# Kernel tuning notes

Hardware: AMD Instinct MI355X
Metric: run time of the kernel (lower is better)

## Reference

```python
import jax, jax.numpy as jnp
import numpy as np

T, HID, D, NQ, NKV = 4096, 2048, 128, 16, 4
THETA = 10000.0


def _rope(x, pos):
    # x: [T, N, D], non-interleaved (rotate_half) RoPE
    half = D // 2
    inv_freq = 1.0 / (THETA ** (jnp.arange(0, half, dtype=jnp.float32) / half))
    freqs = pos.astype(jnp.float32)[:, None] * inv_freq[None, :]  # [T, half]
    cos = jnp.cos(freqs)[:, None, :]  # [T, 1, half]
    sin = jnp.sin(freqs)[:, None, :]
    x1, x2 = x[..., :half], x[..., half:]
    return jnp.concatenate([x1 * cos - x2 * sin, x2 * cos + x1 * sin], axis=-1)


def setup_inputs() -> dict:
    key = jax.random.key(0)
    ks = jax.random.split(key, 5)
    s = 0.02
    return {
        "hidden_states": jax.random.normal(ks[0], (T, HID), jnp.float32),
        "wq": jax.random.normal(ks[1], (HID, HID), jnp.float32) * s,
        "wk": jax.random.normal(ks[2], (NKV * D, HID), jnp.float32) * s,
        "wv": jax.random.normal(ks[3], (NKV * D, HID), jnp.float32) * s,
        "wo": jax.random.normal(ks[4], (HID, HID), jnp.float32) * s,
        "position_ids": jnp.arange(T, dtype=jnp.int32),
    }


def reference(hidden_states, wq, wk, wv, wo, position_ids):
    q = (hidden_states @ wq.T).reshape(T, NQ, D)
    k = (hidden_states @ wk.T).reshape(T, NKV, D)
    v = (hidden_states @ wv.T).reshape(T, NKV, D)
    q = _rope(q, position_ids)
    k = _rope(k, position_ids)
    # GQA: share each KV head across NQ//NKV query heads
    rep = NQ // NKV
    k = jnp.repeat(k, rep, axis=1)  # [T, NQ, D]
    v = jnp.repeat(v, rep, axis=1)
    scale = 1.0 / jnp.sqrt(jnp.float32(D))
    scores = jnp.einsum("qhd,khd->hqk", q, k) * scale  # [NQ, T, T]
    causal = jnp.tril(jnp.ones((T, T), dtype=bool))
    scores = jnp.where(causal[None, :, :], scores, jnp.float32(-1e30))
    probs = jax.nn.softmax(scores, axis=-1)
    out = jnp.einsum("hqk,khd->qhd", probs, v).reshape(T, HID)
    return out @ wo.T
```

## Files before the change

### kernel.cpp

```cpp
#include <hip/hip_runtime.h>
#include <hip/hip_bf16.h>
#include <cstdint>

#define T_    4096
#define HID_  2048
#define DH    128
#define NQ_   16
#define NKV_  4
#define QKVW  3072

typedef __attribute__((ext_vector_type(8))) short bf16x8;
typedef __attribute__((ext_vector_type(4))) float f32x4;
typedef __attribute__((ext_vector_type(16))) float f32x16;
typedef __attribute__((ext_vector_type(4))) float f4;
typedef __attribute__((ext_vector_type(4))) short s4;

__device__ __forceinline__ short f2bf(float f) {
  union { float f; unsigned u; } x; x.f = f;
  unsigned r = x.u + 0x7fffu + ((x.u >> 16) & 1u);
  return (short)(r >> 16);
}
__device__ __forceinline__ float bf2f(short s) {
  return __uint_as_float(((unsigned)(unsigned short)s) << 16);
}
__device__ __forceinline__ unsigned pkbf2(float a, float b) {
  union { __hip_bfloat162 h; unsigned u; } c;
  c.h = __float22bfloat162_rn(make_float2(a, b));
  return c.u;
}

__device__ __forceinline__ void gload16(const void* g, void* l) {
  __builtin_amdgcn_global_load_lds(
      (const __attribute__((address_space(1))) unsigned*)g,
      (__attribute__((address_space(3))) unsigned*)l, 16, 0, 0);
}

#define MFMA16(a, b, c) __builtin_amdgcn_mfma_f32_16x16x32_bf16(a, b, c, 0, 0, 0)
#define MFMA32(a, b, c) __builtin_amdgcn_mfma_f32_32x32x16_bf16(a, b, c, 0, 0, 0)

#define Z16 {0.f,0.f,0.f,0.f,0.f,0.f,0.f,0.f,0.f,0.f,0.f,0.f,0.f,0.f,0.f,0.f}
#define SCL2 0.127517432f

#define C_HS 2097152u
#define C_WQ (C_HS + 1048576u)
#define C_WK (C_WQ + 262144u)
#define C_WV (C_WK + 262144u)
#define C_WO (C_WV + 1048576u)
__global__ void cvt_all(const float* __restrict__ hs, const float* __restrict__ wq,
                        const float* __restrict__ wk, const float* __restrict__ wv,
                        const float* __restrict__ wo, short* __restrict__ hs_bf,
                        short* __restrict__ w1_bf, short* __restrict__ wo_bf) {
  const unsigned stride = gridDim.x * blockDim.x;
  for (unsigned i = blockIdx.x * blockDim.x + threadIdx.x; i < C_WO; i += stride) {
    const float* s; short* d; unsigned off;
    if (i < C_HS)      { s = hs; d = hs_bf;           off = i; }
    else if (i < C_WQ) { s = wq; d = w1_bf;           off = i - C_HS; }
    else if (i < C_WK) { s = wk; d = w1_bf + 4194304; off = i - C_WQ; }
    else if (i < C_WV) { s = wv; d = w1_bf + 5242880; off = i - C_WK; }
    else               { s = wo; d = wo_bf;           off = i - C_WV; }
    f4 v = ((const f4*)s)[off];
    s4 o;
    o[0] = f2bf(v[0]); o[1] = f2bf(v[1]); o[2] = f2bf(v[2]); o[3] = f2bf(v[3]);
    ((s4*)d)[off] = o;
  }
}

template <int BF16OUT>
__global__ __launch_bounds__(256) void gemm_bt(const short* __restrict__ A,
                                               const short* __restrict__ B,
                                               void* __restrict__ Cp,
                                               int N, int K) {
  __shared__ short lA[128 * 64];
  __shared__ short lB[128 * 64];
  const int nb = gridDim.x * gridDim.y;
  const int lin = blockIdx.y * gridDim.x + blockIdx.x;
  const int per = nb >> 3;
  const int wg = (lin & 7) * per + (lin >> 3);
  const int bx = wg % gridDim.x;
  const int by = wg / gridDim.x;

  const int tid = threadIdx.x;
  const int lane = tid & 63;
  const int w = tid >> 6;
  const int wr = w >> 1, wc = w & 1;
  const int l15 = lane & 15, l4 = lane >> 4;
  f32x4 acc[4][4];
#pragma unroll
  for (int m = 0; m < 4; m++)
#pragma unroll
    for (int n = 0; n < 4; n++) acc[m][n] = f32x4{0.f, 0.f, 0.f, 0.f};

  const short* Ag = A + (size_t)bx * 128 * K;
  const short* Bg = B + (size_t)by * 128 * K;

  for (int kt = 0; kt < K; kt += 64) {
#pragma unroll
    for (int i = 0; i < 4; ++i) {
      const int cb = i * 256 + w * 64;
      const int c = cb + lane;
      const int row = c >> 3;
      const int x = (c & 7) << 4;
      const int sx = x ^ ((row & 7) << 4);
      gload16(Ag + (size_t)row * K + kt + (sx >> 1), (char*)lA + cb * 16);
      gload16(Bg + (size_t)row * K + kt + (sx >> 1), (char*)lB + cb * 16);
    }
    __syncthreads();
    bf16x8 af[4][2], bfr[4][2];
#pragma unroll
    for (int m = 0; m < 4; m++) {
      const int row = wr * 64 + m * 16 + l15;
      const int sw = (row & 7) << 4;
#pragma unroll
      for (int kk = 0; kk < 2; kk++)
        af[m][kk] = *(const bf16x8*)((const char*)lA + row * 128 + ((kk * 64 + l4 * 16) ^ sw));
    }
#pragma unroll
    for (int n = 0; n < 4; n++) {
      const int row = wc * 64 + n * 16 + l15;
      const int sw = (row & 7) << 4;
#pragma unroll
      for (int kk = 0; kk < 2; kk++)
        bfr[n][kk] = *(const bf16x8*)((const char*)lB + row * 128 + ((kk * 64 + l4 * 16) ^ sw));
    }
#pragma unroll
    for (int m = 0; m < 4; m++)
#pragma unroll
      for (int n = 0; n < 4; n++) {
        acc[m][n] = MFMA16(af[m][0], bfr[n][0], acc[m][n]);
        acc[m][n] = MFMA16(af[m][1], bfr[n][1], acc[m][n]);
      }
    __syncthreads();
  }

  const int r0 = bx * 128 + wr * 64;
  const int c0 = by * 128 + wc * 64;
#pragma unroll
  for (int m = 0; m < 4; m++)
#pragma unroll
    for (int n = 0; n < 4; n++)
#pragma unroll
      for (int r = 0; r < 4; r++) {
        const int row = r0 + m * 16 + l4 * 4 + r;
        const int col = c0 + n * 16 + l15;
        if (BF16OUT)
          ((short*)Cp)[(size_t)row * N + col] = f2bf(acc[m][n][r]);
        else
          ((float*)Cp)[(size_t)row * N + col] = acc[m][n][r];
      }
}

__global__ void rope_k(short* __restrict__ qkv, const int* __restrict__ pos) {
  __shared__ float cs[64], sn[64];
  const int row = blockIdx.x;
  const int tid = threadIdx.x;
  if (tid < 64) {
    const float fp = (float)pos[row];
    const float freq = fp * powf(10000.0f, -(float)tid * (1.0f / 64.0f));
    cs[tid] = cosf(freq);
    sn[tid] = sinf(freq);
  }
  __syncthreads();
  const int p = tid * 4;
  const int head = p >> 6;
  const int d0 = p & 63;
  const int col0 = (head < NQ_) ? head * DH : HID_ + (head - NQ_) * DH;
  const float scl = (head < NQ_) ? SCL2 : 1.0f;
  short* q = qkv + (size_t)row * QKVW + col0 + d0;
  s4 x1 = *(const s4*)q;
  s4 x2 = *(const s4*)(q + 64);
  s4 o1, o2;
#pragma unroll
  for (int j = 0; j < 4; j++) {
    const float c = cs[d0 + j], s = sn[d0 + j];
    const float a = bf2f(x1[j]), b = bf2f(x2[j]);
    o1[j] = f2bf((a * c - b * s) * scl);
    o2[j] = f2bf((b * c + a * s) * scl);
  }
  *(s4*)q = o1;
  *(s4*)(q + 64) = o2;
}

#define PRE(j)                                                                      \
  {                                                                                 \
    const int kv0e = (j) * 128, kv0o = (j) * 128 + 64;                              \
    _Pragma("unroll") for (int i = 0; i < 2; i++) {                                 \
      const int idx = i * 512 + tid;                                                \
      const int row = idx >> 4, e = (idx & 15) << 3;                                \
      kre[i] = *(const bf16x8*)(kbase + (size_t)(kv0e + row) * QKVW + e);           \
      kro[i] = *(const bf16x8*)(kbase + (size_t)(kv0o + row) * QKVW + e);           \
    }                                                                               \
    {                                                                               \
      const int rp = tid >> 4, e = (tid & 15) << 3;                                 \
      vre[0] = *(const bf16x8*)(vbase + (size_t)(kv0e + 2 * rp) * QKVW + e);        \
      vre[1] = *(const bf16x8*)(vbase + (size_t)(kv0e + 2 * rp + 1) * QKVW + e);    \
      vro[0] = *(const bf16x8*)(vbase + (size_t)(kv0o + 2 * rp) * QKVW + e);        \
      vro[1] = *(const bf16x8*)(vbase + (size_t)(kv0o + 2 * rp + 1) * QKVW + e);    \
    }                                                                               \
  }

#define WRITEBUF(bufp)                                                          \
  {                                                                             \
    char* sKe_ = (bufp);                                                        \
    char* sKo_ = (bufp) + 16384;                                                \
    char* sVe_ = (bufp) + 32768;                                                \
    char* sVo_ = (bufp) + 49152;                                                \
    _Pragma("unroll") for (int i = 0; i < 2; i++) {                             \
      const int idx = i * 512 + tid;                                            \
      const int row = idx >> 4, e16 = (idx & 15) << 4;                          \
      const int swz = (((row >> 3) ^ row) & 7) << 4;                            \
      *(bf16x8*)(sKe_ + row * 256 + (e16 ^ swz)) = kre[i];                      \
      *(bf16x8*)(sKo_ + row * 256 + (e16 ^ swz)) = kro[i];                      \
    }                                                                           \
    {                                                                           \
      const int rp = tid >> 4, e = (tid & 15) << 3;                             \
      const int rp2 = (rp & ~6) | ((rp & 2) << 1) | ((rp & 4) >> 1);            \
      _Pragma("unroll") for (int jj = 0; jj < 8; jj++) {                        \
        const int d = e + jj;                                                   \
        const int swz = (((d >> 3) ^ d) & 7) << 4;                              \
        const unsigned pe = ((unsigned)(unsigned short)vre[0][jj]) |            \
                            (((unsigned)(unsigned short)vre[1][jj]) << 16);     \
        const unsigned po = ((unsigned)(unsigned short)vro[0][jj]) |            \
                            (((unsigned)(unsigned short)vro[1][jj]) << 16);     \
        *(unsigned*)(sVe_ + d * 128 + ((rp2 * 4) ^ swz)) = pe;                  \
        *(unsigned*)(sVo_ + d * 128 + ((rp2 * 4) ^ swz)) = po;                  \
      }                                                                         \
    }                                                                           \
  }

__global__ __launch_bounds__(512) void attn_k(const short* __restrict__ qkv,
                                              short* __restrict__ aout) {
  __shared__ __align__(16) char smem[67584];
  float* ml = (float*)(smem + 65536);

  const int lin = blockIdx.x;
  const int xcd = lin & 7;
  const int slot = lin >> 3;
  const int kvh = xcd >> 1;
  const int qb = 127 - (slot * 2 + (xcd & 1));
  const int tid = threadIdx.x, lane = tid & 63, w = tid >> 6;
  const int head = w & 3, sp = w >> 2;
  const int hi = lane >> 5, l31 = lane & 31;
  const int h = kvh * 4 + head;

  const short* kbase = qkv + HID_ + kvh * DH;
  const short* vbase = qkv + HID_ + NKV_ * DH + kvh * DH;
  const int spoff = sp ? 16384 : 0;

  const int qrow0 = qb * 32;
  const int ntiles = qb / 2 + 1;
  const int nsuper = (ntiles + 1) >> 1;
  const int myq = qrow0 + l31;

  bf16x8 qf[8];
  {
    const short* qp = qkv + (size_t)myq * QKVW + h * DH + hi * 8;
#pragma unroll
    for (int c = 0; c < 8; c++) qf[c] = *(const bf16x8*)(qp + c * 16);
  }
  f32x16 o[4] = {Z16, Z16, Z16, Z16};
  float m = -3e38f, l = 0.f;

  bf16x8 kre[2], kro[2], vre[2], vro[2];
  PRE(0)

  for (int j = 0; j < nsuper; ++j) {
    __syncthreads();
    WRITEBUF(smem)
    __syncthreads();
    if (j + 1 < nsuper) PRE(j + 1)
    const char* bK = smem + spoff;
    const char* bV = smem + 32768 + spoff;

    const int t = 2 * j + sp;
    if (t < ntiles) {
      const int kv0 = t * 64;
      f32x16 s0 = Z16, s1 = Z16;
      const int sw0 = (((l31 >> 3) ^ l31) & 7) << 4;
      const int r1 = 32 + l31;
      const int sw1 = (((r1 >> 3) ^ r1) & 7) << 4;
      __builtin_amdgcn_s_setprio(1);
#pragma unroll
      for (int c = 0; c < 8; c++) {
        const int co = c * 32 + hi * 16;
        const bf16x8 k0 = *(const bf16x8*)(bK + l31 * 256 + (co ^ sw0));
        const bf16x8 k1 = *(const bf16x8*)(bK + r1 * 256 + (co ^ sw1));
        s0 = MFMA32(k0, qf[c], s0);
        s1 = MFMA32(k1, qf[c], s1);
      }
      __builtin_amdgcn_s_setprio(0);
      float sv0[16], sv1[16];
      if (t == ntiles - 1) {
#pragma unroll
        for (int r = 0; r < 16; r++) {
          const int kk = (r & 3) + 8 * (r >> 2) + 4 * hi;
          sv0[r] = (kv0 + kk <= myq) ? s0[r] : -1e30f;
          sv1[r] = (kv0 + 32 + kk <= myq) ? s1[r] : -1e30f;
        }
      } else {
#pragma unroll
        for (int r = 0; r < 16; r++) {
          sv0[r] = s0[r];
          sv1[r] = s1[r];
        }
      }
      float mx[8];
#pragma unroll
      for (int r = 0; r < 8; r++)
        mx[r] = fmaxf(fmaxf(sv0[r], sv0[r + 8]), fmaxf(sv1[r], sv1[r + 8]));
#pragma unroll
      for (int st = 4; st > 0; st >>= 1)
#pragma unroll
        for (int r = 0; r < 4; r++)
          if (r < st) mx[r] = fmaxf(mx[r], mx[r + st]);
      float pm = fmaxf(mx[0], __shfl_xor(mx[0], 32));
      if (__any(pm > m + 11.5f)) {
        const float mn = fmaxf(m, pm);
        const float al = exp2f(m - mn);
        m = mn;
        l *= al;
#pragma unroll
        for (int r = 0; r < 16; r++) {
          const float ar = __shfl(al, (r & 3) + 8 * (r >> 2) + 4 * hi);
#pragma unroll
          for (int dt = 0; dt < 4; dt++) o[dt][r] *= ar;
        }
      }
      float pv0[16], pv1[16];
#pragma unroll
      for (int r = 0; r < 16; r++) {
        pv0[r] = exp2f(sv0[r] - m);
        pv1[r] = exp2f(sv1[r] - m);
      }
      float sum[8];
#pragma unroll
      for (int r = 0; r < 8; r++)
        sum[r] = (pv0[r] + pv0[r + 8]) + (pv1[r] + pv1[r + 8]);
#pragma unroll
      for (int st = 4; st > 0; st >>= 1)
#pragma unroll
        for (int r = 0; r < 4; r++)
          if (r < st) sum[r] = sum[r] + sum[r + st];
      l += sum[0] + __shfl_xor(sum[0], 32);

      unsigned W0[8], W1[8];
#pragma unroll
      for (int i = 0; i < 8; i++) {
        W0[i] = pkbf2(pv0[2 * i], pv0[2 * i + 1]);
        W1[i] = pkbf2(pv1[2 * i], pv1[2 * i + 1]);
      }
#pragma unroll
      for (int kt = 0; kt < 2; kt++) {
#pragma unroll
        for (int hc = 0; hc < 2; hc++) {
          union { unsigned u[4]; bf16x8 v; } fr;
#pragma unroll
          for (int mm = 0; mm < 4; mm++)
            fr.u[mm] = kt ? W1[hc * 4 + mm] : W0[hc * 4 + mm];
          const int ko = kt * 64 + hc * 32 + hi * 16;
          __builtin_amdgcn_s_setprio(1);
#pragma unroll
          for (int dt = 0; dt < 4; dt++) {
            const int row = dt * 32 + l31;
            const int swz = (((row >> 3) ^ row) & 7) << 4;
            const bf16x8 vf = *(const bf16x8*)(bV + row * 128 + (ko ^ swz));
            o[dt] = MFMA32(fr.v, vf, o[dt]);
          }
          __builtin_amdgcn_s_setprio(0);
        }
      }
    }
  }

  if (lane < 32) {
    ml[((head * 2 + sp) * 2) * 32 + lane] = m;
    ml[((head * 2 + sp) * 2 + 1) * 32 + lane] = l;
  }
  __syncthreads();
  const float mo = ml[((head * 2 + (1 - sp)) * 2) * 32 + l31];
  const float lo = ml[((head * 2 + (1 - sp)) * 2 + 1) * 32 + l31];
  const float M = fmaxf(m, mo);
  const float aown = exp2f(m - M);
  const float ltot = l * aown + lo * exp2f(mo - M);
#pragma unroll
  for (int r = 0; r < 16; r++) {
    const float ar = __shfl(aown, (r & 3) + 8 * (r >> 2) + 4 * hi);
#pragma unroll
    for (int dt = 0; dt < 4; dt++) o[dt][r] *= ar;
  }
  float* Ob = (float*)smem + head * 4096;
  if (sp == 1) {
#pragma unroll
    for (int r = 0; r < 16; r++) {
      const int q = (r & 3) + 8 * (r >> 2) + 4 * hi;
#pragma unroll
      for (int dt = 0; dt < 4; dt++) Ob[q * 128 + dt * 32 + l31] = o[dt][r];
    }
  }
  __syncthreads();
  if (sp == 0) {
    const float ri = 1.0f / ltot;
#pragma unroll
    for (int r = 0; r < 16; r++) {
      const float rr = __shfl(ri, (r & 3) + 8 * (r >> 2) + 4 * hi);
      const int q = (r & 3) + 8 * (r >> 2) + 4 * hi;
#pragma unroll
      for (int dt = 0; dt < 4; dt++) {
        const float val = (o[dt][r] + Ob[q * 128 + dt * 32 + l31]) * rr;
        aout[(size_t)(qrow0 + q) * HID_ + h * DH + dt * 32 + l31] = f2bf(val);
      }
    }
  }
}

extern "C" void kernel_launch(void* const* d_in, const int* in_sizes, int n_in,
                              void* d_out, int out_size, void* d_ws, size_t ws_size,
                              hipStream_t stream) {
  const float* hs = (const float*)d_in[0];
  const float* wq = (const float*)d_in[1];
  const float* wk = (const float*)d_in[2];
  const float* wv = (const float*)d_in[3];
  const float* wo = (const float*)d_in[4];
  const int* pos = (const int*)d_in[5];
  float* out = (float*)d_out;

  const size_t SZ_HS = (size_t)T_ * HID_;
  const size_t SZ_WQ = (size_t)HID_ * HID_;
  const size_t SZ_W1 = (size_t)QKVW * HID_;
  const size_t SZ_QKV = (size_t)T_ * QKVW;

  short* hs_bf = (short*)d_ws;
  short* w1_bf = hs_bf + SZ_HS;
  short* wo_bf = w1_bf + SZ_W1;
  short* qkv = wo_bf + SZ_WQ;
  short* attn = qkv + SZ_QKV;

  cvt_all<<<2048, 256, 0, stream>>>(hs, wq, wk, wv, wo, hs_bf, w1_bf, wo_bf);

  gemm_bt<1><<<dim3(T_ / 128, QKVW / 128), 256, 0, stream>>>(hs_bf, w1_bf, qkv, QKVW, HID_);

  rope_k<<<dim3(T_), 320, 0, stream>>>(qkv, pos);

  attn_k<<<dim3(512), 512, 0, stream>>>(qkv, attn);

  gemm_bt<0><<<dim3(T_ / 128, HID_ / 128), 256, 0, stream>>>(attn, wo_bf, out, HID_, HID_);
}
```

Baseline: 256.1 us.

## Drop split-KV within attention block; use 4 waves each iterating all KV tiles

Result: slower. 293.9 us (+14.7%).

```diff
diff --git a/kernel.cpp b/kernel.cpp
--- a/kernel.cpp
+++ b/kernel.cpp
@@ -180,36 +180,33 @@
   *(s4*)(q + 64) = o2;
 }
 
-#define PRE(j)                                                                      \
+
+#define PRE(tt)                                                                     \
   {                                                                                 \
-    const int kv0e = (j) * 128, kv0o = (j) * 128 + 64;                              \
-    _Pragma("unroll") for (int i = 0; i < 2; i++) {                                 \
-      const int idx = i * 512 + tid;                                                \
-      const int row = idx >> 4, e = (idx & 15) << 3;                                \
-      kre[i] = *(const bf16x8*)(kbase + (size_t)(kv0e + row) * QKVW + e);           \
-      kro[i] = *(const bf16x8*)(kbase + (size_t)(kv0o + row) * QKVW + e);           \
+    const int kv0p = (tt) * 64;                                                     \
+    _Pragma("unroll") for (int i = 0; i < 4; i++) {                                 \
+      const int c = i * 256 + tid;                                                  \
+      const int row = c >> 4, e = (c & 15) << 3;                                    \
+      kr[i] = *(const bf16x8*)(kbase + (size_t)(kv0p + row) * QKVW + e);            \
     }                                                                               \
     {                                                                               \
       const int rp = tid >> 4, e = (tid & 15) << 3;                                 \
-      vre[0] = *(const bf16x8*)(vbase + (size_t)(kv0e + 2 * rp) * QKVW + e);        \
-      vre[1] = *(const bf16x8*)(vbase + (size_t)(kv0e + 2 * rp + 1) * QKVW + e);    \
-      vro[0] = *(const bf16x8*)(vbase + (size_t)(kv0o + 2 * rp) * QKVW + e);        \
-      vro[1] = *(const bf16x8*)(vbase + (size_t)(kv0o + 2 * rp + 1) * QKVW + e);    \
+      vr[0] = *(const bf16x8*)(vbase + (size_t)(kv0p + 2 * rp) * QKVW + e);         \
+      vr[1] = *(const bf16x8*)(vbase + (size_t)(kv0p + 2 * rp + 1) * QKVW + e);     \
+      vr[2] = *(const bf16x8*)(vbase + (size_t)(kv0p + 2 * rp + 32) * QKVW + e);    \
+      vr[3] = *(const bf16x8*)(vbase + (size_t)(kv0p + 2 * rp + 33) * QKVW + e);    \
     }                                                                               \
   }
 
-#define WRITEBUF(bufp)                                                          \
+#define WRITEBUF()                                                              \
   {                                                                             \
-    char* sKe_ = (bufp);                                                        \
-    char* sKo_ = (bufp) + 16384;                                                \
-    char* sVe_ = (bufp) + 32768;                                                \
-    char* sVo_ = (bufp) + 49152;                                                \
-    _Pragma("unroll") for (int i = 0; i < 2; i++) {                             \
-      const int idx = i * 512 + tid;                                            \
-      const int row = idx >> 4, e16 = (idx & 15) << 4;                          \
+    char* sK_ = smem;                                                           \
+    char* sV_ = smem + 16384;                                                   \
+    _Pragma("unroll") for (int i = 0; i < 4; i++) {                             \
+      const int c = i * 256 + tid;                                              \
+      const int row = c >> 4, e16 = (c & 15) << 4;                              \
       const int swz = (((row >> 3) ^ row) & 7) << 4;                            \
-      *(bf16x8*)(sKe_ + row * 256 + (e16 ^ swz)) = kre[i];                      \
-      *(bf16x8*)(sKo_ + row * 256 + (e16 ^ swz)) = kro[i];                      \
+      *(bf16x8*)(sK_ + row * 256 + (e16 ^ swz)) = kr[i];                        \
     }                                                                           \
     {                                                                           \
       const int rp = tid >> 4, e = (tid & 15) << 3;                             \
@@ -217,38 +214,34 @@
       _Pragma("unroll") for (int jj = 0; jj < 8; jj++) {                        \
         const int d = e + jj;                                                   \
         const int swz = (((d >> 3) ^ d) & 7) << 4;                              \
-        const unsigned pe = ((unsigned)(unsigned short)vre[0][jj]) |            \
-                            (((unsigned)(unsigned short)vre[1][jj]) << 16);     \
-        const unsigned po = ((unsigned)(unsigned short)vro[0][jj]) |            \
-                            (((unsigned)(unsigned short)vro[1][jj]) << 16);     \
-        *(unsigned*)(sVe_ + d * 128 + ((rp2 * 4) ^ swz)) = pe;                  \
-        *(unsigned*)(sVo_ + d * 128 + ((rp2 * 4) ^ swz)) = po;                  \
+        const unsigned p0 = ((unsigned)(unsigned short)vr[0][jj]) |             \
+                            (((unsigned)(unsigned short)vr[1][jj]) << 16);      \
+        const unsigned p1 = ((unsigned)(unsigned short)vr[2][jj]) |             \
+                            (((unsigned)(unsigned short)vr[3][jj]) << 16);      \
+        *(unsigned*)(sV_ + d * 128 + ((rp2 * 4) ^ swz)) = p0;                   \
+        *(unsigned*)(sV_ + d * 128 + (((rp2 + 16) * 4) ^ swz)) = p1;            \
       }                                                                         \
     }                                                                           \
   }
 
-__global__ __launch_bounds__(512) void attn_k(const short* __restrict__ qkv,
+__global__ __launch_bounds__(256) void attn_k(const short* __restrict__ qkv,
                                               short* __restrict__ aout) {
-  __shared__ __align__(16) char smem[67584];
-  float* ml = (float*)(smem + 65536);
+  __shared__ __align__(16) char smem[32768];
 
   const int lin = blockIdx.x;
   const int xcd = lin & 7;
   const int slot = lin >> 3;
   const int kvh = xcd >> 1;
   const int qb = 127 - (slot * 2 + (xcd & 1));
-  const int tid = threadIdx.x, lane = tid & 63, w = tid >> 6;
-  const int head = w & 3, sp = w >> 2;
+  const int tid = threadIdx.x, lane = tid & 63, head = tid >> 6;
   const int hi = lane >> 5, l31 = lane & 31;
   const int h = kvh * 4 + head;
 
   const short* kbase = qkv + HID_ + kvh * DH;
   const short* vbase = qkv + HID_ + NKV_ * DH + kvh * DH;
-  const int spoff = sp ? 16384 : 0;
 
   const int qrow0 = qb * 32;
   const int ntiles = qb / 2 + 1;
-  const int nsuper = (ntiles + 1) >> 1;
   const int myq = qrow0 + l31;
 
   bf16x8 qf[8];
@@ -260,155 +253,122 @@
   f32x16 o[4] = {Z16, Z16, Z16, Z16};
   float m = -3e38f, l = 0.f;
 
-  bf16x8 kre[2], kro[2], vre[2], vro[2];
+  bf16x8 kr[4], vr[4];
   PRE(0)
 
-  for (int j = 0; j < nsuper; ++j) {
+  for (int t = 0; t < ntiles; ++t) {
     __syncthreads();
-    WRITEBUF(smem)
+    WRITEBUF()
     __syncthreads();
-    if (j + 1 < nsuper) PRE(j + 1)
-    const char* bK = smem + spoff;
-    const char* bV = smem + 32768 + spoff;
-
-    const int t = 2 * j + sp;
-    if (t < ntiles) {
-      const int kv0 = t * 64;
-      f32x16 s0 = Z16, s1 = Z16;
-      const int sw0 = (((l31 >> 3) ^ l31) & 7) << 4;
-      const int r1 = 32 + l31;
-      const int sw1 = (((r1 >> 3) ^ r1) & 7) << 4;
-      __builtin_amdgcn_s_setprio(1);
-#pragma unroll
-      for (int c = 0; c < 8; c++) {
-        const int co = c * 32 + hi * 16;
-        const bf16x8 k0 = *(const bf16x8*)(bK + l31 * 256 + (co ^ sw0));
-        const bf16x8 k1 = *(const bf16x8*)(bK + r1 * 256 + (co ^ sw1));
-        s0 = MFMA32(k0, qf[c], s0);
-        s1 = MFMA32(k1, qf[c], s1);
-      }
-      __builtin_amdgcn_s_setprio(0);
-      float sv0[16], sv1[16];
-      if (t == ntiles - 1) {
-#pragma unroll
-        for (int r = 0; r < 16; r++) {
-          const int kk = (r & 3) + 8 * (r >> 2) + 4 * hi;
-          sv0[r] = (kv0 + kk <= myq) ? s0[r] : -1e30f;
-          sv1[r] = (kv0 + 32 + kk <= myq) ? s1[r] : -1e30f;
+    if (t + 1 < ntiles) PRE(t + 1)
+    const char* bK = smem;
+    const char* bV = smem + 16384;
+    const int kv0 = t * 64;
+
+    f32x16 s0 = Z16, s1 = Z16;
+    const int sw0 = (((l31 >> 3) ^ l31) & 7) << 4;
+    const int r1 = 32 + l31;
+    const int sw1 = (((r1 >> 3) ^ r1) & 7) << 4;
+    __builtin_amdgcn_s_setprio(1);
+#pragma unroll
+    for (int c = 0; c < 8; c++) {
+      const int co = c * 32 + hi * 16;
+      const bf16x8 k0 = *(const bf16x8*)(bK + l31 * 256 + (co ^ sw0));
+      const bf16x8 k1 = *(const bf16x8*)(bK + r1 * 256 + (co ^ sw1));
+      s0 = MFMA32(k0, qf[c], s0);
+      s1 = MFMA32(k1, qf[c], s1);
+    }
+    __builtin_amdgcn_s_setprio(0);
+    float sv0[16], sv1[16];
+    if (t == ntiles - 1) {
+#pragma unroll
+      for (int r = 0; r < 16; r++) {
+        const int kk = (r & 3) + 8 * (r >> 2) + 4 * hi;
+        sv0[r] = (kv0 + kk <= myq) ? s0[r] : -1e30f;
+        sv1[r] = (kv0 + 32 + kk <= myq) ? s1[r] : -1e30f;
+      }
+    } else {
+#pragma unroll
+      for (int r = 0; r < 16; r++) {
+        sv0[r] = s0[r];
+        sv1[r] = s1[r];
+      }
+    }
+    float mx[8];
+#pragma unroll
+    for (int r = 0; r < 8; r++)
+      mx[r] = fmaxf(fmaxf(sv0[r], sv0[r + 8]), fmaxf(sv1[r], sv1[r + 8]));
+#pragma unroll
+    for (int st = 4; st > 0; st >>= 1)
+#pragma unroll
+      for (int r = 0; r < 4; r++)
+        if (r < st) mx[r] = fmaxf(mx[r], mx[r + st]);
+    float pm = fmaxf(mx[0], __shfl_xor(mx[0], 32));
+    if (__any(pm > m + 11.5f)) {
+      const float mn = fmaxf(m, pm);
+      const float al = exp2f(m - mn);
+      m = mn;
+      l *= al;
+#pragma unroll
+      for (int r = 0; r < 16; r++) {
+        const float ar = __shfl(al, (r & 3) + 8 * (r >> 2) + 4 * hi);
+#pragma unroll
+        for (int dt = 0; dt < 4; dt++) o[dt][r] *= ar;
+      }
+    }
+    float pv0[16], pv1[16];
+#pragma unroll
+    for (int r = 0; r < 16; r++) {
+      pv0[r] = exp2f(sv0[r] - m);
+      pv1[r] = exp2f(sv1[r] - m);
+    }
+    float sum[8];
+#pragma unroll
+    for (int r = 0; r < 8; r++)
+      sum[r] = (pv0[r] + pv0[r + 8]) + (pv1[r] + pv1[r + 8]);
+#pragma unroll
+    for (int st = 4; st > 0; st >>= 1)
+#pragma unroll
+      for (int r = 0; r < 4; r++)
+        if (r < st) sum[r] = sum[r] + sum[r + st];
+    l += sum[0] + __shfl_xor(sum[0], 32);
+
+    unsigned W0[8], W1[8];
+#pragma unroll
+    for (int i = 0; i < 8; i++) {
+      W0[i] = pkbf2(pv0[2 * i], pv0[2 * i + 1]);
+      W1[i] = pkbf2(pv1[2 * i], pv1[2 * i + 1]);
+    }
+#pragma unroll
+    for (int kt = 0; kt < 2; kt++) {
+#pragma unroll
+      for (int hc = 0; hc < 2; hc++) {
+        union { unsigned u[4]; bf16x8 v; } fr;
+#pragma unroll
+        for (int mm = 0; mm < 4; mm++)
+          fr.u[mm] = kt ? W1[hc * 4 + mm] : W0[hc * 4 + mm];
+        const int ko = kt * 64 + hc * 32 + hi * 16;
+        __builtin_amdgcn_s_setprio(1);
+#pragma unroll
+        for (int dt = 0; dt < 4; dt++) {
+          const int row = dt * 32 + l31;
+          const int swz = (((row >> 3) ^ row) & 7) << 4;
+          const bf16x8 vf = *(const bf16x8*)(bV + row * 128 + (ko ^ swz));
+          o[dt] = MFMA32(fr.v, vf, o[dt]);
         }
-      } else {
-#pragma unroll
-        for (int r = 0; r < 16; r++) {
-          sv0[r] = s0[r];
-          sv1[r] = s1[r];
-        }
-      }
-      float mx[8];
-#pragma unroll
-      for (int r = 0; r < 8; r++)
-        mx[r] = fmaxf(fmaxf(sv0[r], sv0[r + 8]), fmaxf(sv1[r], sv1[r + 8]));
-#pragma unroll
-      for (int st = 4; st > 0; st >>= 1)
-#pragma unroll
-        for (int r = 0; r < 4; r++)
-          if (r < st) mx[r] = fmaxf(mx[r], mx[r + st]);
-      float pm = fmaxf(mx[0], __shfl_xor(mx[0], 32));
-      if (__any(pm > m + 11.5f)) {
-        const float mn = fmaxf(m, pm);
-        const float al = exp2f(m - mn);
-        m = mn;
-        l *= al;
-#pragma unroll
-        for (int r = 0; r < 16; r++) {
-          const float ar = __shfl(al, (r & 3) + 8 * (r >> 2) + 4 * hi);
-#pragma unroll
-          for (int dt = 0; dt < 4; dt++) o[dt][r] *= ar;
-        }
-      }
-      float pv0[16], pv1[16];
-#pragma unroll
-      for (int r = 0; r < 16; r++) {
-        pv0[r] = exp2f(sv0[r] - m);
-        pv1[r] = exp2f(sv1[r] - m);
-      }
-      float sum[8];
-#pragma unroll
-      for (int r = 0; r < 8; r++)
-        sum[r] = (pv0[r] + pv0[r + 8]) + (pv1[r] + pv1[r + 8]);
-#pragma unroll
-      for (int st = 4; st > 0; st >>= 1)
-#pragma unroll
-        for (int r = 0; r < 4; r++)
-          if (r < st) sum[r] = sum[r] + sum[r + st];
-      l += sum[0] + __shfl_xor(sum[0], 32);
-
-      unsigned W0[8], W1[8];
-#pragma unroll
-      for (int i = 0; i < 8; i++) {
-        W0[i] = pkbf2(pv0[2 * i], pv0[2 * i + 1]);
-        W1[i] = pkbf2(pv1[2 * i], pv1[2 * i + 1]);
-      }
-#pragma unroll
-      for (int kt = 0; kt < 2; kt++) {
-#pragma unroll
-        for (int hc = 0; hc < 2; hc++) {
-          union { unsigned u[4]; bf16x8 v; } fr;
-#pragma unroll
-          for (int mm = 0; mm < 4; mm++)
-            fr.u[mm] = kt ? W1[hc * 4 + mm] : W0[hc * 4 + mm];
-          const int ko = kt * 64 + hc * 32 + hi * 16;
-          __builtin_amdgcn_s_setprio(1);
-#pragma unroll
-          for (int dt = 0; dt < 4; dt++) {
-            const int row = dt * 32 + l31;
-            const int swz = (((row >> 3) ^ row) & 7) << 4;
-            const bf16x8 vf = *(const bf16x8*)(bV + row * 128 + (ko ^ swz));
-            o[dt] = MFMA32(fr.v, vf, o[dt]);
-          }
-          __builtin_amdgcn_s_setprio(0);
-        }
-      }
-    }
-  }
-
-  if (lane < 32) {
-    ml[((head * 2 + sp) * 2) * 32 + lane] = m;
-    ml[((head * 2 + sp) * 2 + 1) * 32 + lane] = l;
-  }
-  __syncthreads();
-  const float mo = ml[((head * 2 + (1 - sp)) * 2) * 32 + l31];
-  const float lo = ml[((head * 2 + (1 - sp)) * 2 + 1) * 32 + l31];
-  const float M = fmaxf(m, mo);
-  const float aown = exp2f(m - M);
-  const float ltot = l * aown + lo * exp2f(mo - M);
+        __builtin_amdgcn_s_setprio(0);
+      }
+    }
+  }
+
+  const float ri = 1.0f / l;
 #pragma unroll
   for (int r = 0; r < 16; r++) {
-    const float ar = __shfl(aown, (r & 3) + 8 * (r >> 2) + 4 * hi);
-#pragma unroll
-    for (int dt = 0; dt < 4; dt++) o[dt][r] *= ar;
-  }
-  float* Ob = (float*)smem + head * 4096;
-  if (sp == 1) {
-#pragma unroll
-    for (int r = 0; r < 16; r++) {
-      const int q = (r & 3) + 8 * (r >> 2) + 4 * hi;
-#pragma unroll
-      for (int dt = 0; dt < 4; dt++) Ob[q * 128 + dt * 32 + l31] = o[dt][r];
-    }
-  }
-  __syncthreads();
-  if (sp == 0) {
-    const float ri = 1.0f / ltot;
-#pragma unroll
-    for (int r = 0; r < 16; r++) {
-      const float rr = __shfl(ri, (r & 3) + 8 * (r >> 2) + 4 * hi);
-      const int q = (r & 3) + 8 * (r >> 2) + 4 * hi;
-#pragma unroll
-      for (int dt = 0; dt < 4; dt++) {
-        const float val = (o[dt][r] + Ob[q * 128 + dt * 32 + l31]) * rr;
-        aout[(size_t)(qrow0 + q) * HID_ + h * DH + dt * 32 + l31] = f2bf(val);
-      }
-    }
+    const int q = (r & 3) + 8 * (r >> 2) + 4 * hi;
+    const float rr = __shfl(ri, q);
+#pragma unroll
+    for (int dt = 0; dt < 4; dt++)
+      aout[(size_t)(qrow0 + q) * HID_ + h * DH + dt * 32 + l31] = f2bf(o[dt][r] * rr);
   }
 }
 
@@ -440,7 +400,7 @@
 
   rope_k<<<dim3(T_), 320, 0, stream>>>(qkv, pos);
 
-  attn_k<<<dim3(512), 512, 0, stream>>>(qkv, attn);
+  attn_k<<<dim3(512), 256, 0, stream>>>(qkv, attn);
 
   gemm_bt<0><<<dim3(T_ / 128, HID_ / 128), 256, 0, stream>>>(attn, wo_bf, out, HID_, HID_);
 }
```
